# Optimization experiments

Hardware: AMD Instinct MI355X
Metric: run time of the kernel (lower is better)

Reference implementation:

```python
import jax, jax.numpy as jnp
import numpy as np

N = 50000      # nodes (== nbr_nodes)
E = 800000     # edges
D_IN = 128
D_H = 128
D_OUT = 47
NOISE_RATE = 0.1
EPS = 1e-12


def _lin_init(key, out_f, in_f):
    # rough Glorot-style init for a PyG Linear weight [out_f, in_f]
    s = 1.0 / np.sqrt(in_f)
    return jax.random.uniform(key, (out_f, in_f), jnp.float32, -s, s)


def setup_inputs() -> dict:
    key = jax.random.key(0)
    ks = jax.random.split(key, 13)
    inp = {
        "x": jax.random.normal(ks[0], (N, D_IN), jnp.float32),
        "edge_index": jax.random.randint(ks[1], (2, E), 0, N, dtype=jnp.int32),
        "noise": jax.random.normal(ks[2], (N, D_IN), jnp.float32),
        # layer 0: in -> hidden
        "W_l0": _lin_init(ks[3], D_H, D_IN),
        "b_l0": jnp.zeros((D_H,), jnp.float32),
        "W_r0": _lin_init(ks[4], D_H, D_IN),
        # layer 1: hidden -> hidden
        "W_l1": _lin_init(ks[5], D_H, D_H),
        "b_l1": jnp.zeros((D_H,), jnp.float32),
        "W_r1": _lin_init(ks[6], D_H, D_H),
        # layer 2: hidden -> out
        "W_l2": _lin_init(ks[7], D_OUT, D_H),
        "b_l2": jnp.zeros((D_OUT,), jnp.float32),
        "W_r2": _lin_init(ks[8], D_OUT, D_H),
    }
    return inp


def _sage_conv(x, src, dst, W_l, b_l, W_r):
    # PyG SAGEConv with mean aggregation:
    #   out_i = W_l @ mean_{j in N(i)} x_j + b_l + W_r @ x_i
    msg = x[src]                                              # [E, d] gather
    ssum = jax.ops.segment_sum(msg, dst, num_segments=N)      # [N, d]
    cnt = jax.ops.segment_sum(jnp.ones((src.shape[0], 1), x.dtype), dst,
                              num_segments=N)                 # [N, 1]
    agg = ssum / jnp.maximum(cnt, 1.0)                        # mean; 0 for isolated nodes
    return agg @ W_l.T + b_l + x @ W_r.T


def _branch(x, src, dst, params):
    # stacked SAGEConv; relu after all but last layer; dropout is identity (eval mode)
    h = None
    n_layers = len(params)
    for i, (W_l, b_l, W_r) in enumerate(params):
        x = _sage_conv(x, src, dst, W_l, b_l, W_r)
        if i != n_layers - 1:
            x = jax.nn.relu(x)
            h = x
    return h, jax.nn.log_softmax(x, axis=1), x


def _add_noise(x, noise):
    # n_id=None path: x + sign(x) * F.normalize(noise, dim=1) * noise_rate
    norm = jnp.sqrt(jnp.sum(noise * noise, axis=1, keepdims=True))
    unit = noise / jnp.maximum(norm, EPS)
    return x + jnp.sign(x) * unit * NOISE_RATE


def reference(x, edge_index, noise,
              W_l0, b_l0, W_r0, W_l1, b_l1, W_r1, W_l2, b_l2, W_r2):
    src, dst = edge_index[0], edge_index[1]
    params = [(W_l0, b_l0, W_r0), (W_l1, b_l1, W_r1), (W_l2, b_l2, W_r2)]
    h_p, y_p, z_p = _branch(x, src, dst, params)
    h_n, y_n, z_n = _branch(_add_noise(x, noise), src, dst, params)
    return (h_p, y_p, z_p, h_n, y_n, z_n)
```

## Files before the change

kernel.cpp:

```cpp
#include <hip/hip_runtime.h>
#include <math.h>


typedef unsigned int uint;
typedef unsigned short ushort;
typedef unsigned char uchar;
typedef short bf16x8 __attribute__((ext_vector_type(8)));
typedef float f32x4 __attribute__((ext_vector_type(4)));

__device__ __forceinline__ ushort f2b(float f) {
  union { float f; uint u; } v; v.f = f;
  uint u = v.u;
  return (ushort)((u + 0x7FFFu + ((u >> 16) & 1u)) >> 16);
}
__device__ __forceinline__ float b2f_lo(uint u) {
  union { uint u; float f; } v; v.u = u << 16; return v.f;
}
__device__ __forceinline__ float b2f_hi(uint u) {
  union { uint u; float f; } v; v.u = u & 0xFFFF0000u; return v.f;
}

#if __has_builtin(__builtin_amdgcn_cvt_f32_fp8)
__device__ __forceinline__ float dec8_0(uint u) {
  return __builtin_amdgcn_cvt_f32_fp8(u, 0);
}
__device__ __forceinline__ float dec8_1(uint u) {
  return __builtin_amdgcn_cvt_f32_fp8(u, 1);
}
#else
__device__ __forceinline__ float dec8_b(uint b) {
  uint s = (b >> 7) & 1u, ex = (b >> 3) & 0xFu, m = b & 7u;
  union { uint u; float f; } v;
  if (ex == 0) {
    v.f = (float)m * 0.001953125f;
    v.u |= s << 31;
    return v.f;
  }
  v.u = (s << 31) | ((ex + 120u) << 23) | (m << 20);
  return v.f;
}
__device__ __forceinline__ float dec8_0(uint u) { return dec8_b(u & 0xFFu); }
__device__ __forceinline__ float dec8_1(uint u) { return dec8_b((u >> 8) & 0xFFu); }
#endif

#if __has_builtin(__builtin_amdgcn_cvt_pk_fp8_f32)
__device__ __forceinline__ uchar enc8(float f) {
  return (uchar)(__builtin_amdgcn_cvt_pk_fp8_f32(f, f, 0u, false) & 0xFFu);
}
#else
__device__ __forceinline__ uchar enc8(float f) {
  union { float f; uint u; } v; v.f = f;
  uint s = v.u >> 31;
  uint a = v.u & 0x7FFFFFFFu;
  if (a >= 0x43E00000u) return (uchar)((s << 7) | 0x7Eu);
  if (a < 0x3C800000u) {
    float q = fabsf(f) * 512.0f;
    uint m = (uint)(q + 0.5f);
    return (uchar)((s << 7) | m);
  }
  uint r = a + 0x00080000u;
  if (r >= 0x43E00000u) return (uchar)((s << 7) | 0x7Eu);
  uint ex = (r >> 23) - 120u;
  uint m = (r >> 20) & 7u;
  return (uchar)((s << 7) | (ex << 3) | m);
}
#endif

__global__ __launch_bounds__(256) void count_kernel(
    const int* __restrict__ dst, int* __restrict__ cnt, int E) {
  int e = blockIdx.x * blockDim.x + threadIdx.x;
  if (e >= E) return;
  atomicAdd(&cnt[dst[e]], 1);
}

__global__ __launch_bounds__(256) void scan_blocks(
    const int* __restrict__ cnt, int* __restrict__ loc,
    int* __restrict__ bsum, int n) {
  __shared__ int ls[4];
  int t = threadIdx.x;
  int base = blockIdx.x * 1024 + t * 4;
  int v[4];
  int s = 0;
#pragma unroll
  for (int i = 0; i < 4; ++i) {
    v[i] = (base + i < n) ? cnt[base + i] : 0;
    s += v[i];
  }
  int lane = t & 63, wid = t >> 6;
  int ps = s;
#pragma unroll
  for (int d = 1; d < 64; d <<= 1) {
    int o = __shfl_up(ps, d, 64);
    if (lane >= d) ps += o;
  }
  if (lane == 63) ls[wid] = ps;
  __syncthreads();
  if (t == 0) {
    int r = 0;
#pragma unroll
    for (int w = 0; w < 4; ++w) { int x = ls[w]; ls[w] = r; r += x; }
  }
  __syncthreads();
  int run = ps - s + ls[wid];
#pragma unroll
  for (int i = 0; i < 4; ++i) {
    if (base + i < n) loc[base + i] = run;
    run += v[i];
  }
  if (t == 255) bsum[blockIdx.x] = ps + ls[wid];
}

__global__ __launch_bounds__(256) void scan_bsums(int* __restrict__ bsum,
                                                  int nb) {
  __shared__ int ls[4];
  int t = threadIdx.x;
  int v = (t < nb) ? bsum[t] : 0;
  int lane = t & 63, wid = t >> 6;
  int ps = v;
#pragma unroll
  for (int d = 1; d < 64; d <<= 1) {
    int o = __shfl_up(ps, d, 64);
    if (lane >= d) ps += o;
  }
  if (lane == 63) ls[wid] = ps;
  __syncthreads();
  if (t == 0) {
    int r = 0;
#pragma unroll
    for (int w = 0; w < 4; ++w) { int x = ls[w]; ls[w] = r; r += x; }
  }
  __syncthreads();
  if (t < nb) bsum[t] = ps - v + ls[wid];
}

__global__ __launch_bounds__(256) void scan_apply(
    const int* __restrict__ loc, const int* __restrict__ bsum,
    int* __restrict__ off, int* __restrict__ cur, int n, int E) {
  int i = blockIdx.x * 256 + threadIdx.x;
  if (i < n) {
    int v = loc[i] + bsum[i >> 10];
    off[i] = v;
    cur[i] = v;
  }
  if (i == 0) off[n] = E;
}

__global__ __launch_bounds__(256) void fill_kernel(
    const int* __restrict__ src, const int* __restrict__ dst,
    int* __restrict__ cur, int* __restrict__ csr, int E) {
  int e = blockIdx.x * blockDim.x + threadIdx.x;
  if (e >= E) return;
  int pos = atomicAdd(&cur[dst[e]], 1);
  csr[pos] = src[e];
}

__global__ __launch_bounds__(256) void noisy_convert(
    const float* __restrict__ x, const float* __restrict__ noise,
    ushort* __restrict__ XB, int N) {
  int node = (blockIdx.x * blockDim.x + threadIdx.x) >> 6;
  int lane = threadIdx.x & 63;
  if (node >= N) return;
  size_t base = (size_t)node * 128 + 2 * lane;
  float2 nz = *(const float2*)(noise + base);
  float ss = nz.x * nz.x + nz.y * nz.y;
#pragma unroll
  for (int m = 1; m < 64; m <<= 1) ss += __shfl_xor(ss, m, 64);
  float scale = 0.1f / fmaxf(sqrtf(ss), 1e-12f);
  float2 xv = *(const float2*)(x + base);
  float s0 = (xv.x > 0.f) ? 1.f : ((xv.x < 0.f) ? -1.f : 0.f);
  float s1 = (xv.y > 0.f) ? 1.f : ((xv.y < 0.f) ? -1.f : 0.f);
  float n0 = xv.x + s0 * nz.x * scale;
  float n1 = xv.y + s1 * nz.y * scale;
  uint pc = ((uint)f2b(xv.y) << 16) | f2b(xv.x);
  uint pn = ((uint)f2b(n1) << 16) | f2b(n0);
  *(uint*)(XB + (size_t)(2 * node) * 128 + 2 * lane) = pc;
  *(uint*)(XB + (size_t)(2 * node + 1) * 128 + 2 * lane) = pn;
}

__global__ __launch_bounds__(256) void conv_weights(
    const float* __restrict__ Wl0, const float* __restrict__ Wr0,
    const float* __restrict__ Wl1, const float* __restrict__ Wr1,
    const float* __restrict__ Wl2, const float* __restrict__ Wr2,
    ushort* __restrict__ WB0, ushort* __restrict__ WB1,
    ushort* __restrict__ WB2) {
  int i = blockIdx.x * 256 + threadIdx.x;
  if (i < 16384) {
    WB0[i] = f2b(Wl0[i]);
    WB0[16384 + i] = f2b(Wr0[i]);
    WB1[i] = f2b(Wl1[i]);
    WB1[16384 + i] = f2b(Wr1[i]);
  }
  if (i < 6016) {
    WB2[i] = f2b(Wl2[i]);
    WB2[6016 + i] = f2b(Wr2[i]);
  }
}

__global__ __launch_bounds__(512) void gemm_fused(
    const ushort* __restrict__ A, const ushort* __restrict__ W,
    ushort* __restrict__ Pb, float* __restrict__ Rf, int M) {
  __shared__ ushort As[128 * 72];
  __shared__ ushort Ws[256 * 72];
  int tid = threadIdx.x;
  int lane = tid & 63, wid = tid >> 6;
  int wm = wid & 1, wn = wid >> 1;
  int lrow = lane & 15, quad = lane >> 4;
  int row0 = blockIdx.x * 128;

  f32x4 acc[4][4];
#pragma unroll
  for (int mt = 0; mt < 4; ++mt)
#pragma unroll
    for (int nt = 0; nt < 4; ++nt) acc[mt][nt] = (f32x4)(0.f);

  for (int k0 = 0; k0 < 128; k0 += 64) {
    for (int c = tid; c < 128 * 8; c += 512) {
      int r = c >> 3, kc = c & 7;
      int gr = row0 + r;
      uint4 v = make_uint4(0, 0, 0, 0);
      if (gr < M) v = *(const uint4*)(A + (size_t)gr * 128 + k0 + kc * 8);
      *(uint4*)(As + r * 72 + kc * 8) = v;
    }
    for (int c = tid; c < 256 * 8; c += 512) {
      int r = c >> 3, kc = c & 7;
      uint4 v = *(const uint4*)(W + (size_t)r * 128 + k0 + kc * 8);
      *(uint4*)(Ws + r * 72 + kc * 8) = v;
    }
    __syncthreads();
#pragma unroll
    for (int ks = 0; ks < 64; ks += 32) {
      bf16x8 af[4], bw[4];
#pragma unroll
      for (int mt = 0; mt < 4; ++mt)
        af[mt] = *(const bf16x8*)(As + (wm * 64 + mt * 16 + lrow) * 72 + ks + quad * 8);
#pragma unroll
      for (int nt = 0; nt < 4; ++nt)
        bw[nt] = *(const bf16x8*)(Ws + (wn * 64 + nt * 16 + lrow) * 72 + ks + quad * 8);
#pragma unroll
      for (int mt = 0; mt < 4; ++mt)
#pragma unroll
        for (int nt = 0; nt < 4; ++nt)
          acc[mt][nt] = __builtin_amdgcn_mfma_f32_16x16x32_bf16(
              af[mt], bw[nt], acc[mt][nt], 0, 0, 0);
    }
    __syncthreads();
  }
  uchar* Pd = (uchar*)Pb;
  if (wn < 2) {
#pragma unroll
    for (int mt = 0; mt < 4; ++mt) {
#pragma unroll
      for (int nt = 0; nt < 4; ++nt) {
        int col = wn * 64 + nt * 16 + lrow;
#pragma unroll
        for (int rg = 0; rg < 4; rg += 2) {
          int row = row0 + wm * 64 + mt * 16 + quad * 4 + rg;
          if (row >= M) continue;
          int nd = row >> 1;
          float cv = acc[mt][nt][rg];
          float nv = acc[mt][nt][rg + 1];
          ushort cb = f2b(cv);
          float cr = b2f_lo((uint)cb);
          Pb[(size_t)nd * 192 + col] = cb;
          Pd[(size_t)nd * 384 + 256 + col] = enc8(nv - cr);
        }
      }
    }
  } else {
#pragma unroll
    for (int mt = 0; mt < 4; ++mt) {
#pragma unroll
      for (int nt = 0; nt < 4; ++nt) {
        int colR = (wn - 2) * 64 + nt * 16 + lrow;
#pragma unroll
        for (int rg = 0; rg < 4; ++rg) {
          int row = row0 + wm * 64 + mt * 16 + quad * 4 + rg;
          if (row >= M) continue;
          int nd = row >> 1, hf = row & 1;
          Rf[(size_t)nd * 256 + hf * 128 + colR] = acc[mt][nt][rg];
        }
      }
    }
  }
}

__global__ __launch_bounds__(256) void gemm_l2(
    const ushort* __restrict__ A, const ushort* __restrict__ W,
    ushort* __restrict__ Pb, float* __restrict__ Rf, int M) {
  constexpr int NT = 3;
  __shared__ ushort As[128 * 72];
  __shared__ ushort Ws[96 * 72];
  int tid = threadIdx.x;
  int lane = tid & 63, wid = tid >> 6;
  int wm = wid & 1, wn = wid >> 1;
  int lrow = lane & 15, quad = lane >> 4;
  int row0 = blockIdx.x * 128;

  f32x4 acc[4][NT];
#pragma unroll
  for (int mt = 0; mt < 4; ++mt)
#pragma unroll
    for (int nt = 0; nt < NT; ++nt) acc[mt][nt] = (f32x4)(0.f);

  for (int k0 = 0; k0 < 128; k0 += 64) {
    for (int c = tid; c < 128 * 8; c += 256) {
      int r = c >> 3, kc = c & 7;
      int gr = row0 + r;
      uint4 v = make_uint4(0, 0, 0, 0);
      if (gr < M) v = *(const uint4*)(A + (size_t)gr * 128 + k0 + kc * 8);
      *(uint4*)(As + r * 72 + kc * 8) = v;
    }
    for (int c = tid; c < 96 * 8; c += 256) {
      int r = c >> 3, kc = c & 7;
      uint4 v = make_uint4(0, 0, 0, 0);
      if (r < 94) v = *(const uint4*)(W + (size_t)r * 128 + k0 + kc * 8);
      *(uint4*)(Ws + r * 72 + kc * 8) = v;
    }
    __syncthreads();
#pragma unroll
    for (int ks = 0; ks < 64; ks += 32) {
      bf16x8 af[4], bw[NT];
#pragma unroll
      for (int mt = 0; mt < 4; ++mt)
        af[mt] = *(const bf16x8*)(As + (wm * 64 + mt * 16 + lrow) * 72 + ks + quad * 8);
#pragma unroll
      for (int nt = 0; nt < NT; ++nt)
        bw[nt] = *(const bf16x8*)(Ws + (wn * NT * 16 + nt * 16 + lrow) * 72 + ks + quad * 8);
#pragma unroll
      for (int mt = 0; mt < 4; ++mt)
#pragma unroll
        for (int nt = 0; nt < NT; ++nt)
          acc[mt][nt] = __builtin_amdgcn_mfma_f32_16x16x32_bf16(
              af[mt], bw[nt], acc[mt][nt], 0, 0, 0);
    }
    __syncthreads();
  }
#pragma unroll
  for (int mt = 0; mt < 4; ++mt) {
#pragma unroll
    for (int nt = 0; nt < NT; ++nt) {
#pragma unroll
      for (int rg = 0; rg < 4; ++rg) {
        int row = row0 + wm * 64 + mt * 16 + quad * 4 + rg;
        if (row >= M) continue;
        int col = wn * NT * 16 + nt * 16 + lrow;
        int nd = row >> 1, hf = row & 1;
        float v = acc[mt][nt][rg];
        if (col < 47)
          Pb[(size_t)nd * 128 + hf * 64 + col] = f2b(v);
        else if (col < 94)
          Rf[(size_t)nd * 128 + hf * 64 + (col - 47)] = v;
      }
    }
  }
}

template <bool WF32>
__global__ __launch_bounds__(256) void agg_dual128(
    const ushort* __restrict__ P2, const float* __restrict__ R2,
    const float* __restrict__ bias, const int* __restrict__ off,
    const int* __restrict__ csr, float* __restrict__ f0,
    float* __restrict__ f1, ushort* __restrict__ bout, int N) {
  int node = (blockIdx.x * blockDim.x + threadIdx.x) >> 6;
  int lane = threadIdx.x & 63;
  if (node >= N) return;
  const uchar* PB = (const uchar*)P2;
  int b = off[node], e = off[node + 1];
  float ac0 = 0.f, ac1 = 0.f, bc0 = 0.f, bc1 = 0.f;
  float ad0 = 0.f, ad1 = 0.f, bd0 = 0.f, bd1 = 0.f;
  int j = b;
  for (; j + 8 <= e; j += 8) {
    int s0 = csr[j],     s1 = csr[j + 1], s2 = csr[j + 2], s3 = csr[j + 3];
    int s4 = csr[j + 4], s5 = csr[j + 5], s6 = csr[j + 6], s7 = csr[j + 7];
    const uchar* p0 = PB + (size_t)s0 * 384;
    const uchar* p1 = PB + (size_t)s1 * 384;
    const uchar* p2 = PB + (size_t)s2 * 384;
    const uchar* p3 = PB + (size_t)s3 * 384;
    const uchar* p4 = PB + (size_t)s4 * 384;
    const uchar* p5 = PB + (size_t)s5 * 384;
    const uchar* p6 = PB + (size_t)s6 * 384;
    const uchar* p7 = PB + (size_t)s7 * 384;
    uint c0 = *(const uint*)(p0 + 4 * lane);
    uint c1 = *(const uint*)(p1 + 4 * lane);
    uint c2 = *(const uint*)(p2 + 4 * lane);
    uint c3 = *(const uint*)(p3 + 4 * lane);
    uint c4 = *(const uint*)(p4 + 4 * lane);
    uint c5 = *(const uint*)(p5 + 4 * lane);
    uint c6 = *(const uint*)(p6 + 4 * lane);
    uint c7 = *(const uint*)(p7 + 4 * lane);
    uint d0 = *(const ushort*)(p0 + 256 + 2 * lane);
    uint d1 = *(const ushort*)(p1 + 256 + 2 * lane);
    uint d2 = *(const ushort*)(p2 + 256 + 2 * lane);
    uint d3 = *(const ushort*)(p3 + 256 + 2 * lane);
    uint d4 = *(const ushort*)(p4 + 256 + 2 * lane);
    uint d5 = *(const ushort*)(p5 + 256 + 2 * lane);
    uint d6 = *(const ushort*)(p6 + 256 + 2 * lane);
    uint d7 = *(const ushort*)(p7 + 256 + 2 * lane);
    ac0 += b2f_lo(c0) + b2f_lo(c1) + b2f_lo(c2) + b2f_lo(c3);
    ac1 += b2f_hi(c0) + b2f_hi(c1) + b2f_hi(c2) + b2f_hi(c3);
    bc0 += b2f_lo(c4) + b2f_lo(c5) + b2f_lo(c6) + b2f_lo(c7);
    bc1 += b2f_hi(c4) + b2f_hi(c5) + b2f_hi(c6) + b2f_hi(c7);
    ad0 += dec8_0(d0) + dec8_0(d1) + dec8_0(d2) + dec8_0(d3);
    ad1 += dec8_1(d0) + dec8_1(d1) + dec8_1(d2) + dec8_1(d3);
    bd0 += dec8_0(d4) + dec8_0(d5) + dec8_0(d6) + dec8_0(d7);
    bd1 += dec8_1(d4) + dec8_1(d5) + dec8_1(d6) + dec8_1(d7);
  }
  if (j + 4 <= e) {
    int s0 = csr[j], s1 = csr[j + 1], s2 = csr[j + 2], s3 = csr[j + 3];
    const uchar* p0 = PB + (size_t)s0 * 384;
    const uchar* p1 = PB + (size_t)s1 * 384;
    const uchar* p2 = PB + (size_t)s2 * 384;
    const uchar* p3 = PB + (size_t)s3 * 384;
    uint c0 = *(const uint*)(p0 + 4 * lane);
    uint c1 = *(const uint*)(p1 + 4 * lane);
    uint c2 = *(const uint*)(p2 + 4 * lane);
    uint c3 = *(const uint*)(p3 + 4 * lane);
    uint d0 = *(const ushort*)(p0 + 256 + 2 * lane);
    uint d1 = *(const ushort*)(p1 + 256 + 2 * lane);
    uint d2 = *(const ushort*)(p2 + 256 + 2 * lane);
    uint d3 = *(const ushort*)(p3 + 256 + 2 * lane);
    ac0 += b2f_lo(c0) + b2f_lo(c1) + b2f_lo(c2) + b2f_lo(c3);
    ac1 += b2f_hi(c0) + b2f_hi(c1) + b2f_hi(c2) + b2f_hi(c3);
    ad0 += dec8_0(d0) + dec8_0(d1) + dec8_0(d2) + dec8_0(d3);
    ad1 += dec8_1(d0) + dec8_1(d1) + dec8_1(d2) + dec8_1(d3);
    j += 4;
  }
  for (; j < e; ++j) {
    const uchar* p0 = PB + (size_t)csr[j] * 384;
    uint c0 = *(const uint*)(p0 + 4 * lane);
    uint d0 = *(const ushort*)(p0 + 256 + 2 * lane);
    ac0 += b2f_lo(c0);
    ac1 += b2f_hi(c0);
    ad0 += dec8_0(d0);
    ad1 += dec8_1(d0);
  }
  ac0 += bc0; ac1 += bc1; ad0 += bd0; ad1 += bd1;
  float an0 = ac0 + ad0, an1 = ac1 + ad1;
  float invd = 1.f / (float)max(e - b, 1);
  float2 rc = *(const float2*)(R2 + (size_t)node * 256 + 2 * lane);
  float2 rn = *(const float2*)(R2 + (size_t)node * 256 + 128 + 2 * lane);
  float2 bb = *(const float2*)(bias + 2 * lane);
  float oc0 = fmaxf(ac0 * invd + bb.x + rc.x, 0.f);
  float oc1 = fmaxf(ac1 * invd + bb.y + rc.y, 0.f);
  float on0 = fmaxf(an0 * invd + bb.x + rn.x, 0.f);
  float on1 = fmaxf(an1 * invd + bb.y + rn.y, 0.f);
  uint pc = ((uint)f2b(oc1) << 16) | f2b(oc0);
  uint pn = ((uint)f2b(on1) << 16) | f2b(on0);
  *(uint*)(bout + (size_t)(2 * node) * 128 + 2 * lane) = pc;
  *(uint*)(bout + (size_t)(2 * node + 1) * 128 + 2 * lane) = pn;
  if (WF32) {
    *(float2*)(f0 + (size_t)node * 128 + 2 * lane) = make_float2(oc0, oc1);
    *(float2*)(f1 + (size_t)node * 128 + 2 * lane) = make_float2(on0, on1);
  }
}

__global__ __launch_bounds__(256) void agg47_dual(
    const ushort* __restrict__ Pz, const float* __restrict__ Rz,
    const float* __restrict__ bias, const int* __restrict__ off,
    const int* __restrict__ csr, float* __restrict__ z0,
    float* __restrict__ z1, float* __restrict__ y0, float* __restrict__ y1,
    int N) {
  int node = (blockIdx.x * blockDim.x + threadIdx.x) >> 6;
  int lane = threadIdx.x & 63;
  if (node >= N) return;
  int half = lane >> 5, lq = lane & 31;
  int c0 = 2 * lq, c1 = 2 * lq + 1;
  bool v0 = c0 < 47, v1 = c1 < 47;
  int b = off[node], e = off[node + 1];
  float a0 = 0.f, a1 = 0.f, d0 = 0.f, d1 = 0.f;
  int j = b;
  for (; j + 8 <= e; j += 8) {
    int s0 = csr[j], s1 = csr[j + 1], s2 = csr[j + 2], s3 = csr[j + 3];
    int s4 = csr[j + 4], s5 = csr[j + 5], s6 = csr[j + 6], s7 = csr[j + 7];
    uint u0 = *(const uint*)(Pz + (size_t)s0 * 128 + 2 * lane);
    uint u1 = *(const uint*)(Pz + (size_t)s1 * 128 + 2 * lane);
    uint u2 = *(const uint*)(Pz + (size_t)s2 * 128 + 2 * lane);
    uint u3 = *(const uint*)(Pz + (size_t)s3 * 128 + 2 * lane);
    uint u4 = *(const uint*)(Pz + (size_t)s4 * 128 + 2 * lane);
    uint u5 = *(const uint*)(Pz + (size_t)s5 * 128 + 2 * lane);
    uint u6 = *(const uint*)(Pz + (size_t)s6 * 128 + 2 * lane);
    uint u7 = *(const uint*)(Pz + (size_t)s7 * 128 + 2 * lane);
    a0 += b2f_lo(u0) + b2f_lo(u1) + b2f_lo(u2) + b2f_lo(u3);
    a1 += b2f_hi(u0) + b2f_hi(u1) + b2f_hi(u2) + b2f_hi(u3);
    d0 += b2f_lo(u4) + b2f_lo(u5) + b2f_lo(u6) + b2f_lo(u7);
    d1 += b2f_hi(u4) + b2f_hi(u5) + b2f_hi(u6) + b2f_hi(u7);
  }
  if (j + 4 <= e) {
    int s0 = csr[j], s1 = csr[j + 1], s2 = csr[j + 2], s3 = csr[j + 3];
    uint u0 = *(const uint*)(Pz + (size_t)s0 * 128 + 2 * lane);
    uint u1 = *(const uint*)(Pz + (size_t)s1 * 128 + 2 * lane);
    uint u2 = *(const uint*)(Pz + (size_t)s2 * 128 + 2 * lane);
    uint u3 = *(const uint*)(Pz + (size_t)s3 * 128 + 2 * lane);
    a0 += b2f_lo(u0) + b2f_lo(u1) + b2f_lo(u2) + b2f_lo(u3);
    a1 += b2f_hi(u0) + b2f_hi(u1) + b2f_hi(u2) + b2f_hi(u3);
    j += 4;
  }
  for (; j < e; ++j) {
    uint u0 = *(const uint*)(Pz + (size_t)csr[j] * 128 + 2 * lane);
    a0 += b2f_lo(u0);
    a1 += b2f_hi(u0);
  }
  a0 += d0; a1 += d1;
  float invd = 1.f / (float)max(e - b, 1);
  float2 rv = *(const float2*)(Rz + (size_t)node * 128 + 2 * lane);
  float za = v0 ? (a0 * invd + bias[c0] + rv.x) : -INFINITY;
  float zb = v1 ? (a1 * invd + bias[c1] + rv.y) : -INFINITY;
  float m = fmaxf(za, zb);
#pragma unroll
  for (int d = 1; d < 32; d <<= 1) m = fmaxf(m, __shfl_xor(m, d, 64));
  float s = (v0 ? __expf(za - m) : 0.f) + (v1 ? __expf(zb - m) : 0.f);
#pragma unroll
  for (int d = 1; d < 32; d <<= 1) s += __shfl_xor(s, d, 64);
  float ls = logf(s) + m;
  float* zo = (half ? z1 : z0) + (size_t)node * 47;
  float* yo = (half ? y1 : y0) + (size_t)node * 47;
  if (v0) { zo[c0] = za; yo[c0] = za - ls; }
  if (v1) { zo[c1] = zb; yo[c1] = zb - ls; }
}

extern "C" void kernel_launch(void* const* d_in, const int* in_sizes, int n_in,
                              void* d_out, int out_size, void* d_ws,
                              size_t ws_size, hipStream_t stream) {
  const float* x = (const float*)d_in[0];
  const int* ei = (const int*)d_in[1];
  const float* noise = (const float*)d_in[2];
  const float* Wl0 = (const float*)d_in[3];
  const float* bl0 = (const float*)d_in[4];
  const float* Wr0 = (const float*)d_in[5];
  const float* Wl1 = (const float*)d_in[6];
  const float* bl1 = (const float*)d_in[7];
  const float* Wr1 = (const float*)d_in[8];
  const float* Wl2 = (const float*)d_in[9];
  const float* bl2 = (const float*)d_in[10];
  const float* Wr2 = (const float*)d_in[11];

  const int N = in_sizes[0] / 128;
  const int E = in_sizes[1] / 2;
  const int M = 2 * N;

  float* out = (float*)d_out;
  float* h_p = out;
  float* y_p = h_p + (size_t)N * 128;
  float* z_p = y_p + (size_t)N * 47;
  float* h_n = z_p + (size_t)N * 47;
  float* y_n = h_n + (size_t)N * 128;
  float* z_n = y_n + (size_t)N * 47;

  char* w = (char*)d_ws;
  auto alloc = [&](size_t bytes) {
    void* p = (void*)w;
    w += (bytes + 511) & ~(size_t)511;
    return p;
  };
  ushort* XB = (ushort*)alloc((size_t)M * 128 * 2);
  ushort* Pb = (ushort*)alloc((size_t)N * 384);
  float* Rf = (float*)alloc((size_t)M * 128 * 4);
  ushort* WB0 = (ushort*)alloc(256 * 128 * 2);
  ushort* WB1 = (ushort*)alloc(256 * 128 * 2);
  ushort* WB2 = (ushort*)alloc(94 * 128 * 2);
  int* cnt = (int*)alloc((size_t)N * 4);
  int* off = (int*)alloc((size_t)(N + 1) * 4);
  int* cur = (int*)alloc((size_t)N * 4);
  int* loc = (int*)alloc((size_t)N * 4);
  int* bsum = (int*)alloc((size_t)256 * 4);
  int* csr = (int*)alloc((size_t)E * 4);

  conv_weights<<<(16384 + 255) / 256, 256, 0, stream>>>(
      Wl0, Wr0, Wl1, Wr1, Wl2, Wr2, WB0, WB1, WB2);

  hipMemsetAsync(cnt, 0, (size_t)N * 4, stream);
  int eb = (E + 255) / 256;
  count_kernel<<<eb, 256, 0, stream>>>(ei + E, cnt, E);
  int sb = (N + 1023) / 1024;
  scan_blocks<<<sb, 256, 0, stream>>>(cnt, loc, bsum, N);
  scan_bsums<<<1, 256, 0, stream>>>(bsum, sb);
  scan_apply<<<(N + 255) / 256, 256, 0, stream>>>(loc, bsum, off, cur, N, E);
  fill_kernel<<<eb, 256, 0, stream>>>(ei, ei + E, cur, csr, E);

  int nwb = (N + 3) / 4;
  int rb = (M + 127) / 128;

  noisy_convert<<<nwb, 256, 0, stream>>>(x, noise, XB, N);

  gemm_fused<<<rb, 512, 0, stream>>>(XB, WB0, Pb, Rf, M);
  agg_dual128<false><<<nwb, 256, 0, stream>>>(Pb, Rf, bl0, off, csr, nullptr,
                                              nullptr, XB, N);
  gemm_fused<<<rb, 512, 0, stream>>>(XB, WB1, Pb, Rf, M);
  agg_dual128<true><<<nwb, 256, 0, stream>>>(Pb, Rf, bl1, off, csr, h_p, h_n,
                                             XB, N);
  gemm_l2<<<rb, 256, 0, stream>>>(XB, WB2, Pb, Rf, M);
  agg47_dual<<<nwb, 256, 0, stream>>>(Pb, Rf, bl2, off, csr, z_p, z_n, y_p,
                                      y_n, N);
}
```

Before: 463.7 us.

## Quantize hidden-layer gather payload to fp8 and drop atomics from CSR fill

Hidden-layer projected features for the clean branch are now stored as fp8 instead of bf16, packed with the fp8 noisy delta into 256-byte rows. This cuts the per-edge gather traffic in the two 128-wide aggregation kernels, and those kernels are reorganised so each lane decodes four fp8 values and the noisy half is recovered with a cross-half shuffle. The output layer gets a separate compact bf16+fp8 layout, with one lane per column and dual softmax reductions. CSR construction records each edge's atomic rank during counting, so the fill pass no longer needs a second atomic. The exchange is lower precision on the clean branch and an extra E-sized rank buffer.

```diff
diff --git a/kernel.cpp b/kernel.cpp
--- a/kernel.cpp
+++ b/kernel.cpp
@@ -21,12 +21,10 @@
 }
 
 #if __has_builtin(__builtin_amdgcn_cvt_f32_fp8)
-__device__ __forceinline__ float dec8_0(uint u) {
-  return __builtin_amdgcn_cvt_f32_fp8(u, 0);
-}
-__device__ __forceinline__ float dec8_1(uint u) {
-  return __builtin_amdgcn_cvt_f32_fp8(u, 1);
-}
+__device__ __forceinline__ float dec8_0(uint u) { return __builtin_amdgcn_cvt_f32_fp8(u, 0); }
+__device__ __forceinline__ float dec8_1(uint u) { return __builtin_amdgcn_cvt_f32_fp8(u, 1); }
+__device__ __forceinline__ float dec8_2(uint u) { return __builtin_amdgcn_cvt_f32_fp8(u, 2); }
+__device__ __forceinline__ float dec8_3(uint u) { return __builtin_amdgcn_cvt_f32_fp8(u, 3); }
 #else
 __device__ __forceinline__ float dec8_b(uint b) {
   uint s = (b >> 7) & 1u, ex = (b >> 3) & 0xFu, m = b & 7u;
@@ -41,6 +39,8 @@
 }
 __device__ __forceinline__ float dec8_0(uint u) { return dec8_b(u & 0xFFu); }
 __device__ __forceinline__ float dec8_1(uint u) { return dec8_b((u >> 8) & 0xFFu); }
+__device__ __forceinline__ float dec8_2(uint u) { return dec8_b((u >> 16) & 0xFFu); }
+__device__ __forceinline__ float dec8_3(uint u) { return dec8_b((u >> 24) & 0xFFu); }
 #endif
 
 #if __has_builtin(__builtin_amdgcn_cvt_pk_fp8_f32)
@@ -67,10 +67,11 @@
 #endif
 
 __global__ __launch_bounds__(256) void count_kernel(
-    const int* __restrict__ dst, int* __restrict__ cnt, int E) {
+    const int* __restrict__ dst, int* __restrict__ cnt,
+    int* __restrict__ rank, int E) {
   int e = blockIdx.x * blockDim.x + threadIdx.x;
   if (e >= E) return;
-  atomicAdd(&cnt[dst[e]], 1);
+  rank[e] = atomicAdd(&cnt[dst[e]], 1);
 }
 
 __global__ __launch_bounds__(256) void scan_blocks(
@@ -135,23 +136,19 @@
 
 __global__ __launch_bounds__(256) void scan_apply(
     const int* __restrict__ loc, const int* __restrict__ bsum,
-    int* __restrict__ off, int* __restrict__ cur, int n, int E) {
+    int* __restrict__ off, int n, int E) {
   int i = blockIdx.x * 256 + threadIdx.x;
-  if (i < n) {
-    int v = loc[i] + bsum[i >> 10];
-    off[i] = v;
-    cur[i] = v;
-  }
+  if (i < n) off[i] = loc[i] + bsum[i >> 10];
   if (i == 0) off[n] = E;
 }
 
 __global__ __launch_bounds__(256) void fill_kernel(
     const int* __restrict__ src, const int* __restrict__ dst,
-    int* __restrict__ cur, int* __restrict__ csr, int E) {
+    const int* __restrict__ rank, const int* __restrict__ off,
+    int* __restrict__ csr, int E) {
   int e = blockIdx.x * blockDim.x + threadIdx.x;
   if (e >= E) return;
-  int pos = atomicAdd(&cur[dst[e]], 1);
-  csr[pos] = src[e];
+  csr[off[dst[e]] + rank[e]] = src[e];
 }
 
 __global__ __launch_bounds__(256) void noisy_convert(
@@ -198,7 +195,7 @@
 
 __global__ __launch_bounds__(512) void gemm_fused(
     const ushort* __restrict__ A, const ushort* __restrict__ W,
-    ushort* __restrict__ Pb, float* __restrict__ Rf, int M) {
+    uchar* __restrict__ P8, float* __restrict__ Rf, int M) {
   __shared__ ushort As[128 * 72];
   __shared__ ushort Ws[256 * 72];
   int tid = threadIdx.x;
@@ -245,7 +242,6 @@
     }
     __syncthreads();
   }
-  uchar* Pd = (uchar*)Pb;
   if (wn < 2) {
 #pragma unroll
     for (int mt = 0; mt < 4; ++mt) {
@@ -259,10 +255,10 @@
           int nd = row >> 1;
           float cv = acc[mt][nt][rg];
           float nv = acc[mt][nt][rg + 1];
-          ushort cb = f2b(cv);
-          float cr = b2f_lo((uint)cb);
-          Pb[(size_t)nd * 192 + col] = cb;
-          Pd[(size_t)nd * 384 + 256 + col] = enc8(nv - cr);
+          uchar c8 = enc8(cv);
+          float cr = dec8_0((uint)c8);
+          P8[(size_t)nd * 256 + col] = c8;
+          P8[(size_t)nd * 256 + 128 + col] = enc8(nv - cr);
         }
       }
     }
@@ -286,7 +282,8 @@
 
 __global__ __launch_bounds__(256) void gemm_l2(
     const ushort* __restrict__ A, const ushort* __restrict__ W,
-    ushort* __restrict__ Pb, float* __restrict__ Rf, int M) {
+    ushort* __restrict__ Pzc, uchar* __restrict__ Pzd,
+    float* __restrict__ Rz, int M) {
   constexpr int NT = 3;
   __shared__ ushort As[128 * 72];
   __shared__ ushort Ws[96 * 72];
@@ -339,17 +336,22 @@
   for (int mt = 0; mt < 4; ++mt) {
 #pragma unroll
     for (int nt = 0; nt < NT; ++nt) {
-#pragma unroll
-      for (int rg = 0; rg < 4; ++rg) {
+      int col = wn * NT * 16 + nt * 16 + lrow;
+#pragma unroll
+      for (int rg = 0; rg < 4; rg += 2) {
         int row = row0 + wm * 64 + mt * 16 + quad * 4 + rg;
         if (row >= M) continue;
-        int col = wn * NT * 16 + nt * 16 + lrow;
-        int nd = row >> 1, hf = row & 1;
-        float v = acc[mt][nt][rg];
-        if (col < 47)
-          Pb[(size_t)nd * 128 + hf * 64 + col] = f2b(v);
-        else if (col < 94)
-          Rf[(size_t)nd * 128 + hf * 64 + (col - 47)] = v;
+        int nd = row >> 1;
+        float cv = acc[mt][nt][rg];
+        float nv = acc[mt][nt][rg + 1];
+        if (col < 47) {
+          ushort cb = f2b(cv);
+          Pzc[(size_t)nd * 64 + col] = cb;
+          Pzd[(size_t)nd * 64 + col] = enc8(nv - b2f_lo((uint)cb));
+        } else if (col < 94) {
+          Rz[(size_t)nd * 128 + (col - 47)] = cv;
+          Rz[(size_t)nd * 128 + 64 + (col - 47)] = nv;
+        }
       }
     }
   }
@@ -357,165 +359,179 @@
 
 template <bool WF32>
 __global__ __launch_bounds__(256) void agg_dual128(
-    const ushort* __restrict__ P2, const float* __restrict__ R2,
+    const uchar* __restrict__ P8, const float* __restrict__ R2,
     const float* __restrict__ bias, const int* __restrict__ off,
     const int* __restrict__ csr, float* __restrict__ f0,
     float* __restrict__ f1, ushort* __restrict__ bout, int N) {
   int node = (blockIdx.x * blockDim.x + threadIdx.x) >> 6;
   int lane = threadIdx.x & 63;
   if (node >= N) return;
-  const uchar* PB = (const uchar*)P2;
+  int lq = lane & 31;
   int b = off[node], e = off[node + 1];
-  float ac0 = 0.f, ac1 = 0.f, bc0 = 0.f, bc1 = 0.f;
-  float ad0 = 0.f, ad1 = 0.f, bd0 = 0.f, bd1 = 0.f;
+  float s0 = 0.f, s1 = 0.f, s2 = 0.f, s3 = 0.f;
+  float t0 = 0.f, t1 = 0.f, t2 = 0.f, t3 = 0.f;
   int j = b;
   for (; j + 8 <= e; j += 8) {
-    int s0 = csr[j],     s1 = csr[j + 1], s2 = csr[j + 2], s3 = csr[j + 3];
-    int s4 = csr[j + 4], s5 = csr[j + 5], s6 = csr[j + 6], s7 = csr[j + 7];
-    const uchar* p0 = PB + (size_t)s0 * 384;
-    const uchar* p1 = PB + (size_t)s1 * 384;
-    const uchar* p2 = PB + (size_t)s2 * 384;
-    const uchar* p3 = PB + (size_t)s3 * 384;
-    const uchar* p4 = PB + (size_t)s4 * 384;
-    const uchar* p5 = PB + (size_t)s5 * 384;
-    const uchar* p6 = PB + (size_t)s6 * 384;
-    const uchar* p7 = PB + (size_t)s7 * 384;
-    uint c0 = *(const uint*)(p0 + 4 * lane);
-    uint c1 = *(const uint*)(p1 + 4 * lane);
-    uint c2 = *(const uint*)(p2 + 4 * lane);
-    uint c3 = *(const uint*)(p3 + 4 * lane);
-    uint c4 = *(const uint*)(p4 + 4 * lane);
-    uint c5 = *(const uint*)(p5 + 4 * lane);
-    uint c6 = *(const uint*)(p6 + 4 * lane);
-    uint c7 = *(const uint*)(p7 + 4 * lane);
-    uint d0 = *(const ushort*)(p0 + 256 + 2 * lane);
-    uint d1 = *(const ushort*)(p1 + 256 + 2 * lane);
-    uint d2 = *(const ushort*)(p2 + 256 + 2 * lane);
-    uint d3 = *(const ushort*)(p3 + 256 + 2 * lane);
-    uint d4 = *(const ushort*)(p4 + 256 + 2 * lane);
-    uint d5 = *(const ushort*)(p5 + 256 + 2 * lane);
-    uint d6 = *(const ushort*)(p6 + 256 + 2 * lane);
-    uint d7 = *(const ushort*)(p7 + 256 + 2 * lane);
-    ac0 += b2f_lo(c0) + b2f_lo(c1) + b2f_lo(c2) + b2f_lo(c3);
-    ac1 += b2f_hi(c0) + b2f_hi(c1) + b2f_hi(c2) + b2f_hi(c3);
-    bc0 += b2f_lo(c4) + b2f_lo(c5) + b2f_lo(c6) + b2f_lo(c7);
-    bc1 += b2f_hi(c4) + b2f_hi(c5) + b2f_hi(c6) + b2f_hi(c7);
-    ad0 += dec8_0(d0) + dec8_0(d1) + dec8_0(d2) + dec8_0(d3);
-    ad1 += dec8_1(d0) + dec8_1(d1) + dec8_1(d2) + dec8_1(d3);
-    bd0 += dec8_0(d4) + dec8_0(d5) + dec8_0(d6) + dec8_0(d7);
-    bd1 += dec8_1(d4) + dec8_1(d5) + dec8_1(d6) + dec8_1(d7);
+    int a0 = csr[j],     a1 = csr[j + 1], a2 = csr[j + 2], a3 = csr[j + 3];
+    int a4 = csr[j + 4], a5 = csr[j + 5], a6 = csr[j + 6], a7 = csr[j + 7];
+    uint u0 = *(const uint*)(P8 + (size_t)a0 * 256 + 4 * lane);
+    uint u1 = *(const uint*)(P8 + (size_t)a1 * 256 + 4 * lane);
+    uint u2 = *(const uint*)(P8 + (size_t)a2 * 256 + 4 * lane);
+    uint u3 = *(const uint*)(P8 + (size_t)a3 * 256 + 4 * lane);
+    uint u4 = *(const uint*)(P8 + (size_t)a4 * 256 + 4 * lane);
+    uint u5 = *(const uint*)(P8 + (size_t)a5 * 256 + 4 * lane);
+    uint u6 = *(const uint*)(P8 + (size_t)a6 * 256 + 4 * lane);
+    uint u7 = *(const uint*)(P8 + (size_t)a7 * 256 + 4 * lane);
+    s0 += dec8_0(u0) + dec8_0(u1) + dec8_0(u2) + dec8_0(u3);
+    s1 += dec8_1(u0) + dec8_1(u1) + dec8_1(u2) + dec8_1(u3);
+    s2 += dec8_2(u0) + dec8_2(u1) + dec8_2(u2) + dec8_2(u3);
+    s3 += dec8_3(u0) + dec8_3(u1) + dec8_3(u2) + dec8_3(u3);
+    t0 += dec8_0(u4) + dec8_0(u5) + dec8_0(u6) + dec8_0(u7);
+    t1 += dec8_1(u4) + dec8_1(u5) + dec8_1(u6) + dec8_1(u7);
+    t2 += dec8_2(u4) + dec8_2(u5) + dec8_2(u6) + dec8_2(u7);
+    t3 += dec8_3(u4) + dec8_3(u5) + dec8_3(u6) + dec8_3(u7);
   }
   if (j + 4 <= e) {
-    int s0 = csr[j], s1 = csr[j + 1], s2 = csr[j + 2], s3 = csr[j + 3];
-    const uchar* p0 = PB + (size_t)s0 * 384;
-    const uchar* p1 = PB + (size_t)s1 * 384;
-    const uchar* p2 = PB + (size_t)s2 * 384;
-    const uchar* p3 = PB + (size_t)s3 * 384;
-    uint c0 = *(const uint*)(p0 + 4 * lane);
-    uint c1 = *(const uint*)(p1 + 4 * lane);
-    uint c2 = *(const uint*)(p2 + 4 * lane);
-    uint c3 = *(const uint*)(p3 + 4 * lane);
-    uint d0 = *(const ushort*)(p0 + 256 + 2 * lane);
-    uint d1 = *(const ushort*)(p1 + 256 + 2 * lane);
-    uint d2 = *(const ushort*)(p2 + 256 + 2 * lane);
-    uint d3 = *(const ushort*)(p3 + 256 + 2 * lane);
-    ac0 += b2f_lo(c0) + b2f_lo(c1) + b2f_lo(c2) + b2f_lo(c3);
-    ac1 += b2f_hi(c0) + b2f_hi(c1) + b2f_hi(c2) + b2f_hi(c3);
-    ad0 += dec8_0(d0) + dec8_0(d1) + dec8_0(d2) + dec8_0(d3);
-    ad1 += dec8_1(d0) + dec8_1(d1) + dec8_1(d2) + dec8_1(d3);
+    int a0 = csr[j], a1 = csr[j + 1], a2 = csr[j + 2], a3 = csr[j + 3];
+    uint u0 = *(const uint*)(P8 + (size_t)a0 * 256 + 4 * lane);
+    uint u1 = *(const uint*)(P8 + (size_t)a1 * 256 + 4 * lane);
+    uint u2 = *(const uint*)(P8 + (size_t)a2 * 256 + 4 * lane);
+    uint u3 = *(const uint*)(P8 + (size_t)a3 * 256 + 4 * lane);
+    s0 += dec8_0(u0) + dec8_0(u1) + dec8_0(u2) + dec8_0(u3);
+    s1 += dec8_1(u0) + dec8_1(u1) + dec8_1(u2) + dec8_1(u3);
+    s2 += dec8_2(u0) + dec8_2(u1) + dec8_2(u2) + dec8_2(u3);
+    s3 += dec8_3(u0) + dec8_3(u1) + dec8_3(u2) + dec8_3(u3);
     j += 4;
   }
   for (; j < e; ++j) {
-    const uchar* p0 = PB + (size_t)csr[j] * 384;
-    uint c0 = *(const uint*)(p0 + 4 * lane);
-    uint d0 = *(const ushort*)(p0 + 256 + 2 * lane);
-    ac0 += b2f_lo(c0);
-    ac1 += b2f_hi(c0);
-    ad0 += dec8_0(d0);
-    ad1 += dec8_1(d0);
-  }
-  ac0 += bc0; ac1 += bc1; ad0 += bd0; ad1 += bd1;
-  float an0 = ac0 + ad0, an1 = ac1 + ad1;
+    uint u0 = *(const uint*)(P8 + (size_t)csr[j] * 256 + 4 * lane);
+    s0 += dec8_0(u0);
+    s1 += dec8_1(u0);
+    s2 += dec8_2(u0);
+    s3 += dec8_3(u0);
+  }
+  s0 += t0; s1 += t1; s2 += t2; s3 += t3;
+  float o0 = __shfl_xor(s0, 32, 64);
+  float o1 = __shfl_xor(s1, 32, 64);
+  float o2 = __shfl_xor(s2, 32, 64);
+  float o3 = __shfl_xor(s3, 32, 64);
+  bool hi = lane >= 32;
+  float m0 = hi ? (s0 + o0) : s0;
+  float m1 = hi ? (s1 + o1) : s1;
+  float m2 = hi ? (s2 + o2) : s2;
+  float m3 = hi ? (s3 + o3) : s3;
   float invd = 1.f / (float)max(e - b, 1);
-  float2 rc = *(const float2*)(R2 + (size_t)node * 256 + 2 * lane);
-  float2 rn = *(const float2*)(R2 + (size_t)node * 256 + 128 + 2 * lane);
-  float2 bb = *(const float2*)(bias + 2 * lane);
-  float oc0 = fmaxf(ac0 * invd + bb.x + rc.x, 0.f);
-  float oc1 = fmaxf(ac1 * invd + bb.y + rc.y, 0.f);
-  float on0 = fmaxf(an0 * invd + bb.x + rn.x, 0.f);
-  float on1 = fmaxf(an1 * invd + bb.y + rn.y, 0.f);
-  uint pc = ((uint)f2b(oc1) << 16) | f2b(oc0);
-  uint pn = ((uint)f2b(on1) << 16) | f2b(on0);
-  *(uint*)(bout + (size_t)(2 * node) * 128 + 2 * lane) = pc;
-  *(uint*)(bout + (size_t)(2 * node + 1) * 128 + 2 * lane) = pn;
+  float4 rv = *(const float4*)(R2 + (size_t)node * 256 + 4 * lane);
+  float4 bb = *(const float4*)(bias + 4 * lq);
+  float q0 = fmaxf(m0 * invd + bb.x + rv.x, 0.f);
+  float q1 = fmaxf(m1 * invd + bb.y + rv.y, 0.f);
+  float q2 = fmaxf(m2 * invd + bb.z + rv.z, 0.f);
+  float q3 = fmaxf(m3 * invd + bb.w + rv.w, 0.f);
+  size_t arow = (size_t)(2 * node + (hi ? 1 : 0)) * 128 + 4 * lq;
+  ushort4 pk;
+  pk.x = f2b(q0); pk.y = f2b(q1); pk.z = f2b(q2); pk.w = f2b(q3);
+  *(ushort4*)(bout + arow) = pk;
   if (WF32) {
-    *(float2*)(f0 + (size_t)node * 128 + 2 * lane) = make_float2(oc0, oc1);
-    *(float2*)(f1 + (size_t)node * 128 + 2 * lane) = make_float2(on0, on1);
+    float* dst = (hi ? f1 : f0) + (size_t)node * 128 + 4 * lq;
+    *(float4*)dst = make_float4(q0, q1, q2, q3);
   }
 }
 
 __global__ __launch_bounds__(256) void agg47_dual(
-    const ushort* __restrict__ Pz, const float* __restrict__ Rz,
-    const float* __restrict__ bias, const int* __restrict__ off,
-    const int* __restrict__ csr, float* __restrict__ z0,
-    float* __restrict__ z1, float* __restrict__ y0, float* __restrict__ y1,
-    int N) {
+    const ushort* __restrict__ Pzc, const uchar* __restrict__ Pzd,
+    const float* __restrict__ Rz, const float* __restrict__ bias,
+    const int* __restrict__ off, const int* __restrict__ csr,
+    float* __restrict__ z0, float* __restrict__ z1, float* __restrict__ y0,
+    float* __restrict__ y1, int N) {
   int node = (blockIdx.x * blockDim.x + threadIdx.x) >> 6;
   int lane = threadIdx.x & 63;
   if (node >= N) return;
-  int half = lane >> 5, lq = lane & 31;
-  int c0 = 2 * lq, c1 = 2 * lq + 1;
-  bool v0 = c0 < 47, v1 = c1 < 47;
+  int lq = lane & 31;
   int b = off[node], e = off[node + 1];
-  float a0 = 0.f, a1 = 0.f, d0 = 0.f, d1 = 0.f;
+  float a = 0.f, aa = 0.f;
+  float g0 = 0.f, g1 = 0.f;
+  float h0 = 0.f, h1 = 0.f;
   int j = b;
   for (; j + 8 <= e; j += 8) {
-    int s0 = csr[j], s1 = csr[j + 1], s2 = csr[j + 2], s3 = csr[j + 3];
-    int s4 = csr[j + 4], s5 = csr[j + 5], s6 = csr[j + 6], s7 = csr[j + 7];
-    uint u0 = *(const uint*)(Pz + (size_t)s0 * 128 + 2 * lane);
-    uint u1 = *(const uint*)(Pz + (size_t)s1 * 128 + 2 * lane);
-    uint u2 = *(const uint*)(Pz + (size_t)s2 * 128 + 2 * lane);
-    uint u3 = *(const uint*)(Pz + (size_t)s3 * 128 + 2 * lane);
-    uint u4 = *(const uint*)(Pz + (size_t)s4 * 128 + 2 * lane);
-    uint u5 = *(const uint*)(Pz + (size_t)s5 * 128 + 2 * lane);
-    uint u6 = *(const uint*)(Pz + (size_t)s6 * 128 + 2 * lane);
-    uint u7 = *(const uint*)(Pz + (size_t)s7 * 128 + 2 * lane);
-    a0 += b2f_lo(u0) + b2f_lo(u1) + b2f_lo(u2) + b2f_lo(u3);
-    a1 += b2f_hi(u0) + b2f_hi(u1) + b2f_hi(u2) + b2f_hi(u3);
-    d0 += b2f_lo(u4) + b2f_lo(u5) + b2f_lo(u6) + b2f_lo(u7);
-    d1 += b2f_hi(u4) + b2f_hi(u5) + b2f_hi(u6) + b2f_hi(u7);
+    int a0 = csr[j],     a1 = csr[j + 1], a2 = csr[j + 2], a3 = csr[j + 3];
+    int a4 = csr[j + 4], a5 = csr[j + 5], a6 = csr[j + 6], a7 = csr[j + 7];
+    uint c0 = Pzc[(size_t)a0 * 64 + lane];
+    uint c1 = Pzc[(size_t)a1 * 64 + lane];
+    uint c2 = Pzc[(size_t)a2 * 64 + lane];
+    uint c3 = Pzc[(size_t)a3 * 64 + lane];
+    uint c4 = Pzc[(size_t)a4 * 64 + lane];
+    uint c5 = Pzc[(size_t)a5 * 64 + lane];
+    uint c6 = Pzc[(size_t)a6 * 64 + lane];
+    uint c7 = Pzc[(size_t)a7 * 64 + lane];
+    uint d0 = *(const ushort*)(Pzd + (size_t)a0 * 64 + 2 * lq);
+    uint d1 = *(const ushort*)(Pzd + (size_t)a1 * 64 + 2 * lq);
+    uint d2 = *(const ushort*)(Pzd + (size_t)a2 * 64 + 2 * lq);
+    uint d3 = *(const ushort*)(Pzd + (size_t)a3 * 64 + 2 * lq);
+    uint d4 = *(const ushort*)(Pzd + (size_t)a4 * 64 + 2 * lq);
+    uint d5 = *(const ushort*)(Pzd + (size_t)a5 * 64 + 2 * lq);
+    uint d6 = *(const ushort*)(Pzd + (size_t)a6 * 64 + 2 * lq);
+    uint d7 = *(const ushort*)(Pzd + (size_t)a7 * 64 + 2 * lq);
+    a  += b2f_lo(c0) + b2f_lo(c1) + b2f_lo(c2) + b2f_lo(c3);
+    aa += b2f_lo(c4) + b2f_lo(c5) + b2f_lo(c6) + b2f_lo(c7);
+    g0 += dec8_0(d0) + dec8_0(d1) + dec8_0(d2) + dec8_0(d3);
+    g1 += dec8_1(d0) + dec8_1(d1) + dec8_1(d2) + dec8_1(d3);
+    h0 += dec8_0(d4) + dec8_0(d5) + dec8_0(d6) + dec8_0(d7);
+    h1 += dec8_1(d4) + dec8_1(d5) + dec8_1(d6) + dec8_1(d7);
   }
   if (j + 4 <= e) {
-    int s0 = csr[j], s1 = csr[j + 1], s2 = csr[j + 2], s3 = csr[j + 3];
-    uint u0 = *(const uint*)(Pz + (size_t)s0 * 128 + 2 * lane);
-    uint u1 = *(const uint*)(Pz + (size_t)s1 * 128 + 2 * lane);
-    uint u2 = *(const uint*)(Pz + (size_t)s2 * 128 + 2 * lane);
-    uint u3 = *(const uint*)(Pz + (size_t)s3 * 128 + 2 * lane);
-    a0 += b2f_lo(u0) + b2f_lo(u1) + b2f_lo(u2) + b2f_lo(u3);
-    a1 += b2f_hi(u0) + b2f_hi(u1) + b2f_hi(u2) + b2f_hi(u3);
+    int a0 = csr[j], a1 = csr[j + 1], a2 = csr[j + 2], a3 = csr[j + 3];
+    uint c0 = Pzc[(size_t)a0 * 64 + lane];
+    uint c1 = Pzc[(size_t)a1 * 64 + lane];
+    uint c2 = Pzc[(size_t)a2 * 64 + lane];
+    uint c3 = Pzc[(size_t)a3 * 64 + lane];
+    uint d0 = *(const ushort*)(Pzd + (size_t)a0 * 64 + 2 * lq);
+    uint d1 = *(const ushort*)(Pzd + (size_t)a1 * 64 + 2 * lq);
+    uint d2 = *(const ushort*)(Pzd + (size_t)a2 * 64 + 2 * lq);
+    uint d3 = *(const ushort*)(Pzd + (size_t)a3 * 64 + 2 * lq);
+    a  += b2f_lo(c0) + b2f_lo(c1) + b2f_lo(c2) + b2f_lo(c3);
+    g0 += dec8_0(d0) + dec8_0(d1) + dec8_0(d2) + dec8_0(d3);
+    g1 += dec8_1(d0) + dec8_1(d1) + dec8_1(d2) + dec8_1(d3);
     j += 4;
   }
   for (; j < e; ++j) {
-    uint u0 = *(const uint*)(Pz + (size_t)csr[j] * 128 + 2 * lane);
-    a0 += b2f_lo(u0);
-    a1 += b2f_hi(u0);
-  }
-  a0 += d0; a1 += d1;
+    uint c0 = Pzc[(size_t)csr[j] * 64 + lane];
+    uint d0 = *(const ushort*)(Pzd + (size_t)csr[j] * 64 + 2 * lq);
+    a += b2f_lo(c0);
+    g0 += dec8_0(d0);
+    g1 += dec8_1(d0);
+  }
+  a += aa; g0 += h0; g1 += h1;
+  float dd0 = __shfl(g0, lane >> 1, 64);
+  float dd1 = __shfl(g1, lane >> 1, 64);
+  float dl = (lane & 1) ? dd1 : dd0;
+  bool v = lane < 47;
   float invd = 1.f / (float)max(e - b, 1);
-  float2 rv = *(const float2*)(Rz + (size_t)node * 128 + 2 * lane);
-  float za = v0 ? (a0 * invd + bias[c0] + rv.x) : -INFINITY;
-  float zb = v1 ? (a1 * invd + bias[c1] + rv.y) : -INFINITY;
-  float m = fmaxf(za, zb);
-#pragma unroll
-  for (int d = 1; d < 32; d <<= 1) m = fmaxf(m, __shfl_xor(m, d, 64));
-  float s = (v0 ? __expf(za - m) : 0.f) + (v1 ? __expf(zb - m) : 0.f);
-#pragma unroll
-  for (int d = 1; d < 32; d <<= 1) s += __shfl_xor(s, d, 64);
-  float ls = logf(s) + m;
-  float* zo = (half ? z1 : z0) + (size_t)node * 47;
-  float* yo = (half ? y1 : y0) + (size_t)node * 47;
-  if (v0) { zo[c0] = za; yo[c0] = za - ls; }
-  if (v1) { zo[c1] = zb; yo[c1] = zb - ls; }
+  float rc = Rz[(size_t)node * 128 + lane];
+  float rn = Rz[(size_t)node * 128 + 64 + lane];
+  float bl = v ? bias[lane] : 0.f;
+  float za = v ? (a * invd + bl + rc) : -INFINITY;
+  float zn = v ? ((a + dl) * invd + bl + rn) : -INFINITY;
+  float ma = za, mb = zn;
+#pragma unroll
+  for (int d = 1; d < 64; d <<= 1) {
+    ma = fmaxf(ma, __shfl_xor(ma, d, 64));
+    mb = fmaxf(mb, __shfl_xor(mb, d, 64));
+  }
+  float sa = v ? __expf(za - ma) : 0.f;
+  float sb = v ? __expf(zn - mb) : 0.f;
+#pragma unroll
+  for (int d = 1; d < 64; d <<= 1) {
+    sa += __shfl_xor(sa, d, 64);
+    sb += __shfl_xor(sb, d, 64);
+  }
+  float lsa = logf(sa) + ma;
+  float lsb = logf(sb) + mb;
+  if (v) {
+    z0[(size_t)node * 47 + lane] = za;
+    y0[(size_t)node * 47 + lane] = za - lsa;
+    z1[(size_t)node * 47 + lane] = zn;
+    y1[(size_t)node * 47 + lane] = zn - lsb;
+  }
 }
 
 extern "C" void kernel_launch(void* const* d_in, const int* in_sizes, int n_in,
@@ -553,42 +569,44 @@
     return p;
   };
   ushort* XB = (ushort*)alloc((size_t)M * 128 * 2);
-  ushort* Pb = (ushort*)alloc((size_t)N * 384);
+  uchar* P8 = (uchar*)alloc((size_t)N * 256);
   float* Rf = (float*)alloc((size_t)M * 128 * 4);
   ushort* WB0 = (ushort*)alloc(256 * 128 * 2);
   ushort* WB1 = (ushort*)alloc(256 * 128 * 2);
   ushort* WB2 = (ushort*)alloc(94 * 128 * 2);
   int* cnt = (int*)alloc((size_t)N * 4);
   int* off = (int*)alloc((size_t)(N + 1) * 4);
-  int* cur = (int*)alloc((size_t)N * 4);
+  int* rank = (int*)alloc((size_t)E * 4);
   int* loc = (int*)alloc((size_t)N * 4);
   int* bsum = (int*)alloc((size_t)256 * 4);
   int* csr = (int*)alloc((size_t)E * 4);
+  ushort* Pzc = (ushort*)P8;
+  uchar* Pzd = P8 + (size_t)N * 128;
 
   conv_weights<<<(16384 + 255) / 256, 256, 0, stream>>>(
       Wl0, Wr0, Wl1, Wr1, Wl2, Wr2, WB0, WB1, WB2);
 
   hipMemsetAsync(cnt, 0, (size_t)N * 4, stream);
   int eb = (E + 255) / 256;
-  count_kernel<<<eb, 256, 0, stream>>>(ei + E, cnt, E);
+  count_kernel<<<eb, 256, 0, stream>>>(ei + E, cnt, rank, E);
   int sb = (N + 1023) / 1024;
   scan_blocks<<<sb, 256, 0, stream>>>(cnt, loc, bsum, N);
   scan_bsums<<<1, 256, 0, stream>>>(bsum, sb);
-  scan_apply<<<(N + 255) / 256, 256, 0, stream>>>(loc, bsum, off, cur, N, E);
-  fill_kernel<<<eb, 256, 0, stream>>>(ei, ei + E, cur, csr, E);
+  scan_apply<<<(N + 255) / 256, 256, 0, stream>>>(loc, bsum, off, N, E);
+  fill_kernel<<<eb, 256, 0, stream>>>(ei, ei + E, rank, off, csr, E);
 
   int nwb = (N + 3) / 4;
   int rb = (M + 127) / 128;
 
   noisy_convert<<<nwb, 256, 0, stream>>>(x, noise, XB, N);
 
-  gemm_fused<<<rb, 512, 0, stream>>>(XB, WB0, Pb, Rf, M);
-  agg_dual128<false><<<nwb, 256, 0, stream>>>(Pb, Rf, bl0, off, csr, nullptr,
+  gemm_fused<<<rb, 512, 0, stream>>>(XB, WB0, P8, Rf, M);
+  agg_dual128<false><<<nwb, 256, 0, stream>>>(P8, Rf, bl0, off, csr, nullptr,
                                               nullptr, XB, N);
-  gemm_fused<<<rb, 512, 0, stream>>>(XB, WB1, Pb, Rf, M);
-  agg_dual128<true><<<nwb, 256, 0, stream>>>(Pb, Rf, bl1, off, csr, h_p, h_n,
+  gemm_fused<<<rb, 512, 0, stream>>>(XB, WB1, P8, Rf, M);
+  agg_dual128<true><<<nwb, 256, 0, stream>>>(P8, Rf, bl1, off, csr, h_p, h_n,
                                              XB, N);
-  gemm_l2<<<rb, 256, 0, stream>>>(XB, WB2, Pb, Rf, M);
-  agg47_dual<<<nwb, 256, 0, stream>>>(Pb, Rf, bl2, off, csr, z_p, z_n, y_p,
-                                      y_n, N);
-}
+  gemm_l2<<<rb, 256, 0, stream>>>(XB, WB2, Pzc, Pzd, Rf, M);
+  agg47_dual<<<nwb, 256, 0, stream>>>(Pzc, Pzd, Rf, bl2, off, csr, z_p, z_n,
+                                      y_p, y_n, N);
+}
```

After: 415.9 us. -10.3%, faster.
